# Optimization experiments

Hardware: AMD Instinct MI355X
Metric: run time of the kernel (lower is better)

## Reference

```python
import jax, jax.numpy as jnp
import numpy as np

HIDDEN = 128
HEADS = 8
HEAD_DIM = HIDDEN // HEADS
N_NODES = 50000
N_EDGES = 500000


def setup_inputs() -> dict:
    key = jax.random.key(0)
    ks = jax.random.split(key, 12)
    s = 1.0 / np.sqrt(HIDDEN)
    inp = {
        "edge_state": jax.random.normal(ks[0], (N_NODES, HIDDEN), jnp.float32),
        "lg_edge_index": jax.random.randint(ks[1], (2, N_EDGES), 0, N_NODES, jnp.int64),
        "angle_emb": jax.random.normal(ks[2], (N_EDGES, HIDDEN), jnp.float32),
        # TransformerConv params (PyG layout translated to [in,out])
        "Wq": jax.random.normal(ks[3], (HIDDEN, HIDDEN), jnp.float32) * s,
        "bq": jnp.zeros((HIDDEN,), jnp.float32),
        "Wk": jax.random.normal(ks[4], (HIDDEN, HIDDEN), jnp.float32) * s,
        "bk": jnp.zeros((HIDDEN,), jnp.float32),
        "Wv": jax.random.normal(ks[5], (HIDDEN, HIDDEN), jnp.float32) * s,
        "bv": jnp.zeros((HIDDEN,), jnp.float32),
        "We": jax.random.normal(ks[6], (HIDDEN, HIDDEN), jnp.float32) * s,  # lin_edge, bias=False
        "Wskip": jax.random.normal(ks[7], (HIDDEN, HIDDEN), jnp.float32) * s,
        "bskip": jnp.zeros((HIDDEN,), jnp.float32),
        "Wbeta": jax.random.normal(ks[8], (3 * HIDDEN, 1), jnp.float32) * s,  # lin_beta, bias=False
        "ln_gamma": jnp.ones((HIDDEN,), jnp.float32),
        "ln_beta": jnp.zeros((HIDDEN,), jnp.float32),
    }
    return inp


def reference(edge_state, lg_edge_index, angle_emb, Wq, bq, Wk, bk, Wv, bv, We,
              Wskip, bskip, Wbeta, ln_gamma, ln_beta):
    N = edge_state.shape[0]
    H, D = HEADS, HEAD_DIM
    src = lg_edge_index[0]  # message source j
    dst = lg_edge_index[1]  # message target i

    q = (edge_state @ Wq + bq).reshape(N, H, D)
    k = (edge_state @ Wk + bk).reshape(N, H, D)
    v = (edge_state @ Wv + bv).reshape(N, H, D)
    e = (angle_emb @ We).reshape(-1, H, D)  # [E,H,D]

    k_e = k[src] + e  # [E,H,D]
    v_e = v[src] + e
    alpha = jnp.einsum('ehd,ehd->eh', q[dst], k_e) / jnp.sqrt(jnp.float32(D))  # [E,H]

    # segment softmax over incoming edges of each target node
    m = jax.ops.segment_max(alpha, dst, num_segments=N)  # [N,H]
    a = jnp.exp(alpha - m[dst])
    z = jax.ops.segment_sum(a, dst, num_segments=N)
    attn = a / z[dst]  # [E,H]

    out = jax.ops.segment_sum(attn[:, :, None] * v_e, dst, num_segments=N)  # [N,H,D]
    out = out.reshape(N, H * D)

    # beta-gated skip (root_weight + beta=True)
    x_r = edge_state @ Wskip + bskip
    beta = jax.nn.sigmoid(jnp.concatenate([out, x_r, out - x_r], axis=-1) @ Wbeta)  # [N,1]
    out = beta * x_r + (1.0 - beta) * out

    # LayerNorm
    mu = jnp.mean(out, axis=-1, keepdims=True)
    var = jnp.mean(jnp.square(out - mu), axis=-1, keepdims=True)
    out = (out - mu) / jnp.sqrt(var + 1e-5) * ln_gamma + ln_beta

    return edge_state + jax.nn.relu(out)
```

## Files before the change

kernel.cpp:

```cpp
#include <hip/hip_runtime.h>
#include <math.h>

#define HIDDEN 128
#define HEADS 8
#define HDIM 16

__global__ __launch_bounds__(128) void gemm128(const float* __restrict__ A,
                                               const float* __restrict__ W,
                                               const float* __restrict__ bias,
                                               float* __restrict__ C, int rows) {
    __shared__ float As[32 * 128];
    const int tid = threadIdx.x;
    const int row0 = blockIdx.x * 32;

    const float4* A4 = reinterpret_cast<const float4*>(A);
    float4* As4 = reinterpret_cast<float4*>(As);
#pragma unroll
    for (int i = 0; i < 8; ++i) {
        int idx4 = tid + i * 128;
        int r = idx4 >> 5;
        float4 val = make_float4(0.f, 0.f, 0.f, 0.f);
        if (row0 + r < rows) val = A4[(size_t)(row0 + r) * 32 + (idx4 & 31)];
        As4[idx4] = val;
    }
    __syncthreads();

    const int c0 = (tid & 31) * 4;
    const int r0 = (tid >> 5) * 8;
    float acc[8][4];
#pragma unroll
    for (int i = 0; i < 8; ++i)
#pragma unroll
        for (int j = 0; j < 4; ++j) acc[i][j] = 0.f;

#pragma unroll 4
    for (int k = 0; k < 128; ++k) {
        const float4 w4 = *reinterpret_cast<const float4*>(&W[k * 128 + c0]);
#pragma unroll
        for (int i = 0; i < 8; ++i) {
            float a = As[(r0 + i) * 128 + k];
            acc[i][0] = fmaf(a, w4.x, acc[i][0]);
            acc[i][1] = fmaf(a, w4.y, acc[i][1]);
            acc[i][2] = fmaf(a, w4.z, acc[i][2]);
            acc[i][3] = fmaf(a, w4.w, acc[i][3]);
        }
    }

    float4 b4 = make_float4(0.f, 0.f, 0.f, 0.f);
    if (bias) b4 = *reinterpret_cast<const float4*>(&bias[c0]);
#pragma unroll
    for (int i = 0; i < 8; ++i) {
        int r = row0 + r0 + i;
        if (r < rows) {
            float4 o;
            o.x = acc[i][0] + b4.x;
            o.y = acc[i][1] + b4.y;
            o.z = acc[i][2] + b4.z;
            o.w = acc[i][3] + b4.w;
            reinterpret_cast<float4*>(C)[(size_t)r * 32 + (c0 >> 2)] = o;
        }
    }
}

__global__ void hist_kernel(const int* __restrict__ dst, int* __restrict__ deg, int E) {
    int i = blockIdx.x * blockDim.x + threadIdx.x;
    if (i < E) atomicAdd(&deg[dst[i]], 1);
}

__global__ void scan_blocks(const int* __restrict__ deg, int* __restrict__ incl,
                            int* __restrict__ bsum, int N) {
    __shared__ int s[256];
    int i = blockIdx.x * 256 + threadIdx.x;
    int vdeg = (i < N) ? deg[i] : 0;
    s[threadIdx.x] = vdeg;
    __syncthreads();
    for (int off = 1; off < 256; off <<= 1) {
        int t = (threadIdx.x >= off) ? s[threadIdx.x - off] : 0;
        __syncthreads();
        s[threadIdx.x] += t;
        __syncthreads();
    }
    if (i < N) incl[i] = s[threadIdx.x];
    if (threadIdx.x == 255) bsum[blockIdx.x] = s[255];
}

__global__ void scan_bsum(const int* __restrict__ bsum, int* __restrict__ boff, int nblk) {
    if (blockIdx.x == 0 && threadIdx.x == 0) {
        int run = 0;
        for (int i = 0; i < nblk; ++i) { boff[i] = run; run += bsum[i]; }
    }
}

__global__ void scan_finalize(const int* __restrict__ incl, const int* __restrict__ deg,
                              const int* __restrict__ boff, int* __restrict__ row_start, int N) {
    int i = blockIdx.x * 256 + threadIdx.x;
    if (i < N) row_start[i] = incl[i] - deg[i] + boff[blockIdx.x];
}

__global__ void scatter_kernel(const int* __restrict__ dst, const int* __restrict__ row_start,
                               int* __restrict__ cursor, int* __restrict__ perm, int E) {
    int i = blockIdx.x * blockDim.x + threadIdx.x;
    if (i < E) {
        int d = dst[i];
        int pos = row_start[d] + atomicAdd(&cursor[d], 1);
        perm[pos] = i;
    }
}

__device__ __forceinline__ float block_reduce_sum_128(float val, float* red) {
#pragma unroll
    for (int off = 32; off > 0; off >>= 1) val += __shfl_xor(val, off, 64);
    int wave = threadIdx.x >> 6;
    if ((threadIdx.x & 63) == 0) red[wave] = val;
    __syncthreads();
    float r = red[0] + red[1];
    __syncthreads();
    return r;
}

__global__ __launch_bounds__(128) void node_fused(
    const float* __restrict__ q, const float* __restrict__ kbuf,
    const float* __restrict__ vbuf, const float* __restrict__ ebuf,
    const float* __restrict__ xr, const float* __restrict__ x_in,
    const int* __restrict__ perm, const int* __restrict__ row_start,
    const int* __restrict__ deg, const int* __restrict__ srcIdx,
    const float* __restrict__ Wb, const float* __restrict__ ln_g,
    const float* __restrict__ ln_b, float* __restrict__ out, int N) {
    __shared__ float red[2];
    const int n = blockIdx.x;
    const int tid = threadIdx.x;

    const float qv = q[(size_t)n * HIDDEN + tid];
    const int start = row_start[n];
    const int cnt = deg[n];

    float m = -INFINITY, z = 0.f, acc = 0.f;
    for (int i = 0; i < cnt; ++i) {
        const int eid = perm[start + i];
        const int s = srcIdx[eid];
        const float ev = ebuf[(size_t)eid * HIDDEN + tid];
        const float ke = kbuf[(size_t)s * HIDDEN + tid] + ev;
        const float ve = vbuf[(size_t)s * HIDDEN + tid] + ev;
        float p = qv * ke;
        p += __shfl_xor(p, 1, 16);
        p += __shfl_xor(p, 2, 16);
        p += __shfl_xor(p, 4, 16);
        p += __shfl_xor(p, 8, 16);
        const float alpha = p * 0.25f;
        const float mn = fmaxf(m, alpha);
        const float sc = __expf(m - mn);
        const float w = __expf(alpha - mn);
        z = z * sc + w;
        acc = acc * sc + w * ve;
        m = mn;
    }
    float out_c = (z > 0.f) ? (acc / z) : 0.f;

    const float x_r_c = xr[(size_t)n * HIDDEN + tid];
    float g = out_c * Wb[tid] + x_r_c * Wb[HIDDEN + tid] + (out_c - x_r_c) * Wb[2 * HIDDEN + tid];
    float logit = block_reduce_sum_128(g, red);
    float beta = 1.f / (1.f + __expf(-logit));
    float o2 = beta * x_r_c + (1.f - beta) * out_c;

    float mean = block_reduce_sum_128(o2, red) * (1.f / 128.f);
    float diff = o2 - mean;
    float var = block_reduce_sum_128(diff * diff, red) * (1.f / 128.f);
    float y = diff * rsqrtf(var + 1e-5f) * ln_g[tid] + ln_b[tid];

    out[(size_t)n * HIDDEN + tid] = x_in[(size_t)n * HIDDEN + tid] + fmaxf(y, 0.f);
}

__global__ void zero_out_kernel(float* __restrict__ out, int n) {
    int i = blockIdx.x * blockDim.x + threadIdx.x;
    if (i < n) out[i] = 0.f;
}

extern "C" void kernel_launch(void* const* d_in, const int* in_sizes, int n_in,
                              void* d_out, int out_size, void* d_ws, size_t ws_size,
                              hipStream_t stream) {
    const float* edge_state = (const float*)d_in[0];
    const int* lg_edge_index = (const int*)d_in[1];
    const float* angle_emb = (const float*)d_in[2];
    const float* Wq = (const float*)d_in[3];
    const float* bq = (const float*)d_in[4];
    const float* Wk = (const float*)d_in[5];
    const float* bk = (const float*)d_in[6];
    const float* Wv = (const float*)d_in[7];
    const float* bv = (const float*)d_in[8];
    const float* We = (const float*)d_in[9];
    const float* Wskip = (const float*)d_in[10];
    const float* bskip = (const float*)d_in[11];
    const float* Wbeta = (const float*)d_in[12];
    const float* ln_g = (const float*)d_in[13];
    const float* ln_b = (const float*)d_in[14];

    const int N = in_sizes[0] / HIDDEN;
    const int E = in_sizes[1] / 2;
    const int* srcIdx = lg_edge_index;
    const int* dstIdx = lg_edge_index + E;

    char* ws = (char*)d_ws;
    size_t off = 0;
    auto alloc = [&](size_t bytes) { void* p = ws + off; off = (off + bytes + 255) & ~size_t(255); return p; };
    float* q   = (float*)alloc((size_t)N * HIDDEN * 4);
    float* k   = (float*)alloc((size_t)N * HIDDEN * 4);
    float* v   = (float*)alloc((size_t)N * HIDDEN * 4);
    float* xr  = (float*)alloc((size_t)N * HIDDEN * 4);
    float* e   = (float*)alloc((size_t)E * HIDDEN * 4);
    int* deg       = (int*)alloc((size_t)N * 4);
    int* cursor    = (int*)alloc((size_t)N * 4);
    int* row_start = (int*)alloc((size_t)N * 4);
    int* incl      = (int*)alloc((size_t)N * 4);
    int* perm      = (int*)alloc((size_t)E * 4);
    const int nblkScan = (N + 255) / 256;
    int* bsum = (int*)alloc((size_t)nblkScan * 4);
    int* boff = (int*)alloc((size_t)nblkScan * 4);

    if (off > ws_size) {
        zero_out_kernel<<<(out_size + 255) / 256, 256, 0, stream>>>((float*)d_out, out_size);
        return;
    }

    const int gN = (N + 31) / 32;
    const int gE = (E + 31) / 32;
    gemm128<<<gN, 128, 0, stream>>>(edge_state, Wq, bq, q, N);
    gemm128<<<gN, 128, 0, stream>>>(edge_state, Wk, bk, k, N);
    gemm128<<<gN, 128, 0, stream>>>(edge_state, Wv, bv, v, N);
    gemm128<<<gN, 128, 0, stream>>>(edge_state, Wskip, bskip, xr, N);
    gemm128<<<gE, 128, 0, stream>>>(angle_emb, We, nullptr, e, E);

    hipMemsetAsync(deg, 0, (size_t)N * 4, stream);
    hipMemsetAsync(cursor, 0, (size_t)N * 4, stream);
    const int eb = (E + 255) / 256;
    hist_kernel<<<eb, 256, 0, stream>>>(dstIdx, deg, E);
    scan_blocks<<<nblkScan, 256, 0, stream>>>(deg, incl, bsum, N);
    scan_bsum<<<1, 1, 0, stream>>>(bsum, boff, nblkScan);
    scan_finalize<<<nblkScan, 256, 0, stream>>>(incl, deg, boff, row_start, N);
    scatter_kernel<<<eb, 256, 0, stream>>>(dstIdx, row_start, cursor, perm, E);

    node_fused<<<N, 128, 0, stream>>>(q, k, v, e, xr, edge_state, perm, row_start,
                                      deg, srcIdx, Wbeta, ln_g, ln_b, (float*)d_out, N);
}
```

Before: 915.6 us.

## Scatter edge projections into dst-sorted order and fuse node GEMMs

The edge-projection GEMM now writes its output rows directly into CSR (destination-sorted) order through an inverse permutation, and source indices are pre-sorted. The aggregation kernel can then read edge features contiguously instead of going through perm and srcIdx indirection. The four node GEMMs are merged into one kernel that reuses the shared-memory A tile, and the aggregation loop processes two edges per iteration. In exchange the edge GEMM does scattered row writes, and the sort has to finish before the GEMMs run.

```diff
diff --git a/kernel.cpp b/kernel.cpp
--- a/kernel.cpp
+++ b/kernel.cpp
@@ -5,10 +5,13 @@
 #define HEADS 8
 #define HDIM 16
 
-__global__ __launch_bounds__(128) void gemm128(const float* __restrict__ A,
-                                               const float* __restrict__ W,
-                                               const float* __restrict__ bias,
-                                               float* __restrict__ C, int rows) {
+__global__ __launch_bounds__(128) void gemm_qkvs(
+    const float* __restrict__ A,
+    const float* __restrict__ W0, const float* __restrict__ b0, float* __restrict__ C0,
+    const float* __restrict__ W1, const float* __restrict__ b1, float* __restrict__ C1,
+    const float* __restrict__ W2, const float* __restrict__ b2, float* __restrict__ C2,
+    const float* __restrict__ W3, const float* __restrict__ b3, float* __restrict__ C3,
+    int rows) {
     __shared__ float As[32 * 128];
     const int tid = threadIdx.x;
     const int row0 = blockIdx.x * 32;
@@ -27,37 +30,134 @@
 
     const int c0 = (tid & 31) * 4;
     const int r0 = (tid >> 5) * 8;
+
+    const float* Ws[4] = {W0, W1, W2, W3};
+    const float* bs[4] = {b0, b1, b2, b3};
+    float* Cs[4] = {C0, C1, C2, C3};
+
+    for (int w = 0; w < 4; ++w) {
+        const float* __restrict__ W = Ws[w];
+        float acc[8][4];
+#pragma unroll
+        for (int i = 0; i < 8; ++i)
+#pragma unroll
+            for (int j = 0; j < 4; ++j) acc[i][j] = 0.f;
+
+#pragma unroll 2
+        for (int k0 = 0; k0 < 128; k0 += 4) {
+            const float4 w0 = *reinterpret_cast<const float4*>(&W[(k0 + 0) * 128 + c0]);
+            const float4 w1 = *reinterpret_cast<const float4*>(&W[(k0 + 1) * 128 + c0]);
+            const float4 w2 = *reinterpret_cast<const float4*>(&W[(k0 + 2) * 128 + c0]);
+            const float4 w3 = *reinterpret_cast<const float4*>(&W[(k0 + 3) * 128 + c0]);
+#pragma unroll
+            for (int i = 0; i < 8; ++i) {
+                const float4 a = As4[(r0 + i) * 32 + (k0 >> 2)];
+                acc[i][0] = fmaf(a.x, w0.x, acc[i][0]);
+                acc[i][1] = fmaf(a.x, w0.y, acc[i][1]);
+                acc[i][2] = fmaf(a.x, w0.z, acc[i][2]);
+                acc[i][3] = fmaf(a.x, w0.w, acc[i][3]);
+                acc[i][0] = fmaf(a.y, w1.x, acc[i][0]);
+                acc[i][1] = fmaf(a.y, w1.y, acc[i][1]);
+                acc[i][2] = fmaf(a.y, w1.z, acc[i][2]);
+                acc[i][3] = fmaf(a.y, w1.w, acc[i][3]);
+                acc[i][0] = fmaf(a.z, w2.x, acc[i][0]);
+                acc[i][1] = fmaf(a.z, w2.y, acc[i][1]);
+                acc[i][2] = fmaf(a.z, w2.z, acc[i][2]);
+                acc[i][3] = fmaf(a.z, w2.w, acc[i][3]);
+                acc[i][0] = fmaf(a.w, w3.x, acc[i][0]);
+                acc[i][1] = fmaf(a.w, w3.y, acc[i][1]);
+                acc[i][2] = fmaf(a.w, w3.z, acc[i][2]);
+                acc[i][3] = fmaf(a.w, w3.w, acc[i][3]);
+            }
+        }
+
+        const float4 b4 = *reinterpret_cast<const float4*>(&bs[w][c0]);
+#pragma unroll
+        for (int i = 0; i < 8; ++i) {
+            int r = row0 + r0 + i;
+            if (r < rows) {
+                float4 o;
+                o.x = acc[i][0] + b4.x;
+                o.y = acc[i][1] + b4.y;
+                o.z = acc[i][2] + b4.z;
+                o.w = acc[i][3] + b4.w;
+                reinterpret_cast<float4*>(Cs[w])[(size_t)r * 32 + (c0 >> 2)] = o;
+            }
+        }
+    }
+}
+
+__global__ __launch_bounds__(128) void gemm_e_scatter(
+    const float* __restrict__ A, const float* __restrict__ W,
+    const int* __restrict__ inv_perm, float* __restrict__ C, int rows) {
+    __shared__ float As[32 * 128];
+    __shared__ int rowmap[32];
+    const int tid = threadIdx.x;
+    const int row0 = blockIdx.x * 32;
+
+    if (tid < 32) {
+        int r = row0 + tid;
+        rowmap[tid] = (r < rows) ? inv_perm[r] : -1;
+    }
+    const float4* A4 = reinterpret_cast<const float4*>(A);
+    float4* As4 = reinterpret_cast<float4*>(As);
+#pragma unroll
+    for (int i = 0; i < 8; ++i) {
+        int idx4 = tid + i * 128;
+        int r = idx4 >> 5;
+        float4 val = make_float4(0.f, 0.f, 0.f, 0.f);
+        if (row0 + r < rows) val = A4[(size_t)(row0 + r) * 32 + (idx4 & 31)];
+        As4[idx4] = val;
+    }
+    __syncthreads();
+
+    const int c0 = (tid & 31) * 4;
+    const int r0 = (tid >> 5) * 8;
     float acc[8][4];
 #pragma unroll
     for (int i = 0; i < 8; ++i)
 #pragma unroll
         for (int j = 0; j < 4; ++j) acc[i][j] = 0.f;
 
-#pragma unroll 4
-    for (int k = 0; k < 128; ++k) {
-        const float4 w4 = *reinterpret_cast<const float4*>(&W[k * 128 + c0]);
+#pragma unroll 2
+    for (int k0 = 0; k0 < 128; k0 += 4) {
+        const float4 w0 = *reinterpret_cast<const float4*>(&W[(k0 + 0) * 128 + c0]);
+        const float4 w1 = *reinterpret_cast<const float4*>(&W[(k0 + 1) * 128 + c0]);
+        const float4 w2 = *reinterpret_cast<const float4*>(&W[(k0 + 2) * 128 + c0]);
+        const float4 w3 = *reinterpret_cast<const float4*>(&W[(k0 + 3) * 128 + c0]);
 #pragma unroll
         for (int i = 0; i < 8; ++i) {
-            float a = As[(r0 + i) * 128 + k];
-            acc[i][0] = fmaf(a, w4.x, acc[i][0]);
-            acc[i][1] = fmaf(a, w4.y, acc[i][1]);
-            acc[i][2] = fmaf(a, w4.z, acc[i][2]);
-            acc[i][3] = fmaf(a, w4.w, acc[i][3]);
+            const float4 a = As4[(r0 + i) * 32 + (k0 >> 2)];
+            acc[i][0] = fmaf(a.x, w0.x, acc[i][0]);
+            acc[i][1] = fmaf(a.x, w0.y, acc[i][1]);
+            acc[i][2] = fmaf(a.x, w0.z, acc[i][2]);
+            acc[i][3] = fmaf(a.x, w0.w, acc[i][3]);
+            acc[i][0] = fmaf(a.y, w1.x, acc[i][0]);
+            acc[i][1] = fmaf(a.y, w1.y, acc[i][1]);
+            acc[i][2] = fmaf(a.y, w1.z, acc[i][2]);
+            acc[i][3] = fmaf(a.y, w1.w, acc[i][3]);
+            acc[i][0] = fmaf(a.z, w2.x, acc[i][0]);
+            acc[i][1] = fmaf(a.z, w2.y, acc[i][1]);
+            acc[i][2] = fmaf(a.z, w2.z, acc[i][2]);
+            acc[i][3] = fmaf(a.z, w2.w, acc[i][3]);
+            acc[i][0] = fmaf(a.w, w3.x, acc[i][0]);
+            acc[i][1] = fmaf(a.w, w3.y, acc[i][1]);
+            acc[i][2] = fmaf(a.w, w3.z, acc[i][2]);
+            acc[i][3] = fmaf(a.w, w3.w, acc[i][3]);
         }
     }
 
-    float4 b4 = make_float4(0.f, 0.f, 0.f, 0.f);
-    if (bias) b4 = *reinterpret_cast<const float4*>(&bias[c0]);
 #pragma unroll
     for (int i = 0; i < 8; ++i) {
         int r = row0 + r0 + i;
         if (r < rows) {
+            int tr = rowmap[r0 + i];
             float4 o;
-            o.x = acc[i][0] + b4.x;
-            o.y = acc[i][1] + b4.y;
-            o.z = acc[i][2] + b4.z;
-            o.w = acc[i][3] + b4.w;
-            reinterpret_cast<float4*>(C)[(size_t)r * 32 + (c0 >> 2)] = o;
+            o.x = acc[i][0];
+            o.y = acc[i][1];
+            o.z = acc[i][2];
+            o.w = acc[i][3];
+            reinterpret_cast<float4*>(C)[(size_t)tr * 32 + (c0 >> 2)] = o;
         }
     }
 }
@@ -97,13 +197,15 @@
     if (i < N) row_start[i] = incl[i] - deg[i] + boff[blockIdx.x];
 }
 
-__global__ void scatter_kernel(const int* __restrict__ dst, const int* __restrict__ row_start,
-                               int* __restrict__ cursor, int* __restrict__ perm, int E) {
+__global__ void build_kernel(const int* __restrict__ dst, const int* __restrict__ src,
+                             const int* __restrict__ row_start, int* __restrict__ cursor,
+                             int* __restrict__ inv_perm, int* __restrict__ src_sorted, int E) {
     int i = blockIdx.x * blockDim.x + threadIdx.x;
     if (i < E) {
         int d = dst[i];
         int pos = row_start[d] + atomicAdd(&cursor[d], 1);
-        perm[pos] = i;
+        inv_perm[i] = pos;
+        src_sorted[pos] = src[i];
     }
 }
 
@@ -118,12 +220,20 @@
     return r;
 }
 
+__device__ __forceinline__ float head_dot16(float p) {
+    p += __shfl_xor(p, 1, 16);
+    p += __shfl_xor(p, 2, 16);
+    p += __shfl_xor(p, 4, 16);
+    p += __shfl_xor(p, 8, 16);
+    return p;
+}
+
 __global__ __launch_bounds__(128) void node_fused(
     const float* __restrict__ q, const float* __restrict__ kbuf,
-    const float* __restrict__ vbuf, const float* __restrict__ ebuf,
+    const float* __restrict__ vbuf, const float* __restrict__ e_sorted,
     const float* __restrict__ xr, const float* __restrict__ x_in,
-    const int* __restrict__ perm, const int* __restrict__ row_start,
-    const int* __restrict__ deg, const int* __restrict__ srcIdx,
+    const int* __restrict__ row_start, const int* __restrict__ deg,
+    const int* __restrict__ src_sorted,
     const float* __restrict__ Wb, const float* __restrict__ ln_g,
     const float* __restrict__ ln_b, float* __restrict__ out, int N) {
     __shared__ float red[2];
@@ -135,23 +245,38 @@
     const int cnt = deg[n];
 
     float m = -INFINITY, z = 0.f, acc = 0.f;
-    for (int i = 0; i < cnt; ++i) {
-        const int eid = perm[start + i];
-        const int s = srcIdx[eid];
-        const float ev = ebuf[(size_t)eid * HIDDEN + tid];
-        const float ke = kbuf[(size_t)s * HIDDEN + tid] + ev;
-        const float ve = vbuf[(size_t)s * HIDDEN + tid] + ev;
-        float p = qv * ke;
-        p += __shfl_xor(p, 1, 16);
-        p += __shfl_xor(p, 2, 16);
-        p += __shfl_xor(p, 4, 16);
-        p += __shfl_xor(p, 8, 16);
-        const float alpha = p * 0.25f;
-        const float mn = fmaxf(m, alpha);
+    int i = 0;
+    for (; i + 2 <= cnt; i += 2) {
+        const int p0 = start + i, p1 = start + i + 1;
+        const int s0 = src_sorted[p0], s1 = src_sorted[p1];
+        const float e0 = e_sorted[(size_t)p0 * HIDDEN + tid];
+        const float e1 = e_sorted[(size_t)p1 * HIDDEN + tid];
+        const float k0 = kbuf[(size_t)s0 * HIDDEN + tid] + e0;
+        const float v0 = vbuf[(size_t)s0 * HIDDEN + tid] + e0;
+        const float k1 = kbuf[(size_t)s1 * HIDDEN + tid] + e1;
+        const float v1 = vbuf[(size_t)s1 * HIDDEN + tid] + e1;
+        float d0 = head_dot16(qv * k0) * 0.25f;
+        float d1 = head_dot16(qv * k1) * 0.25f;
+        const float mn = fmaxf(m, fmaxf(d0, d1));
         const float sc = __expf(m - mn);
-        const float w = __expf(alpha - mn);
-        z = z * sc + w;
-        acc = acc * sc + w * ve;
+        const float w0 = __expf(d0 - mn);
+        const float w1 = __expf(d1 - mn);
+        z = z * sc + w0 + w1;
+        acc = acc * sc + w0 * v0 + w1 * v1;
+        m = mn;
+    }
+    if (i < cnt) {
+        const int p0 = start + i;
+        const int s0 = src_sorted[p0];
+        const float e0 = e_sorted[(size_t)p0 * HIDDEN + tid];
+        const float k0 = kbuf[(size_t)s0 * HIDDEN + tid] + e0;
+        const float v0 = vbuf[(size_t)s0 * HIDDEN + tid] + e0;
+        float d0 = head_dot16(qv * k0) * 0.25f;
+        const float mn = fmaxf(m, d0);
+        const float sc = __expf(m - mn);
+        const float w0 = __expf(d0 - mn);
+        z = z * sc + w0;
+        acc = acc * sc + w0 * v0;
         m = mn;
     }
     float out_c = (z > 0.f) ? (acc / z) : 0.f;
@@ -202,16 +327,17 @@
     char* ws = (char*)d_ws;
     size_t off = 0;
     auto alloc = [&](size_t bytes) { void* p = ws + off; off = (off + bytes + 255) & ~size_t(255); return p; };
-    float* q   = (float*)alloc((size_t)N * HIDDEN * 4);
-    float* k   = (float*)alloc((size_t)N * HIDDEN * 4);
-    float* v   = (float*)alloc((size_t)N * HIDDEN * 4);
-    float* xr  = (float*)alloc((size_t)N * HIDDEN * 4);
-    float* e   = (float*)alloc((size_t)E * HIDDEN * 4);
-    int* deg       = (int*)alloc((size_t)N * 4);
-    int* cursor    = (int*)alloc((size_t)N * 4);
-    int* row_start = (int*)alloc((size_t)N * 4);
-    int* incl      = (int*)alloc((size_t)N * 4);
-    int* perm      = (int*)alloc((size_t)E * 4);
+    float* q        = (float*)alloc((size_t)N * HIDDEN * 4);
+    float* k        = (float*)alloc((size_t)N * HIDDEN * 4);
+    float* v        = (float*)alloc((size_t)N * HIDDEN * 4);
+    float* xr       = (float*)alloc((size_t)N * HIDDEN * 4);
+    float* e_sorted = (float*)alloc((size_t)E * HIDDEN * 4);
+    int* deg        = (int*)alloc((size_t)N * 4);
+    int* cursor     = (int*)alloc((size_t)N * 4);
+    int* row_start  = (int*)alloc((size_t)N * 4);
+    int* incl       = (int*)alloc((size_t)N * 4);
+    int* inv_perm   = (int*)alloc((size_t)E * 4);
+    int* src_sorted = (int*)alloc((size_t)E * 4);
     const int nblkScan = (N + 255) / 256;
     int* bsum = (int*)alloc((size_t)nblkScan * 4);
     int* boff = (int*)alloc((size_t)nblkScan * 4);
@@ -220,14 +346,6 @@
         zero_out_kernel<<<(out_size + 255) / 256, 256, 0, stream>>>((float*)d_out, out_size);
         return;
     }
-
-    const int gN = (N + 31) / 32;
-    const int gE = (E + 31) / 32;
-    gemm128<<<gN, 128, 0, stream>>>(edge_state, Wq, bq, q, N);
-    gemm128<<<gN, 128, 0, stream>>>(edge_state, Wk, bk, k, N);
-    gemm128<<<gN, 128, 0, stream>>>(edge_state, Wv, bv, v, N);
-    gemm128<<<gN, 128, 0, stream>>>(edge_state, Wskip, bskip, xr, N);
-    gemm128<<<gE, 128, 0, stream>>>(angle_emb, We, nullptr, e, E);
 
     hipMemsetAsync(deg, 0, (size_t)N * 4, stream);
     hipMemsetAsync(cursor, 0, (size_t)N * 4, stream);
@@ -236,8 +354,15 @@
     scan_blocks<<<nblkScan, 256, 0, stream>>>(deg, incl, bsum, N);
     scan_bsum<<<1, 1, 0, stream>>>(bsum, boff, nblkScan);
     scan_finalize<<<nblkScan, 256, 0, stream>>>(incl, deg, boff, row_start, N);
-    scatter_kernel<<<eb, 256, 0, stream>>>(dstIdx, row_start, cursor, perm, E);
-
-    node_fused<<<N, 128, 0, stream>>>(q, k, v, e, xr, edge_state, perm, row_start,
-                                      deg, srcIdx, Wbeta, ln_g, ln_b, (float*)d_out, N);
-}
+    build_kernel<<<eb, 256, 0, stream>>>(dstIdx, srcIdx, row_start, cursor,
+                                         inv_perm, src_sorted, E);
+
+    const int gN = (N + 31) / 32;
+    const int gE = (E + 31) / 32;
+    gemm_qkvs<<<gN, 128, 0, stream>>>(edge_state,
+                                      Wq, bq, q, Wk, bk, k, Wv, bv, v, Wskip, bskip, xr, N);
+    gemm_e_scatter<<<gE, 128, 0, stream>>>(angle_emb, We, inv_perm, e_sorted, E);
+
+    node_fused<<<N, 128, 0, stream>>>(q, k, v, e_sorted, xr, edge_state, row_start,
+                                      deg, src_sorted, Wbeta, ln_g, ln_b, (float*)d_out, N);
+}
```

Measured after the change: 888.5 us. 1.03x faster.
